# Performance work log

Measured on AMD Instinct MI355X. Metric: run time of the kernel, lower is better.

Reference implementation:

```python
import jax, jax.numpy as jnp
import numpy as np

TAU = 0.8
ALPHA = 0.05
HEBB_LR = 2e-5
NOISE_SCALE = 0.02
SURROGATE = 0.3

@jax.custom_vjp
def spike(v):
    return (v > 0).astype(v.dtype)

def _spike_fwd(v):
    return (v > 0).astype(v.dtype), v

def _spike_bwd(v, g):
    return (g * (SURROGATE * jnp.maximum(1.0 - jnp.abs(v), 0.0)),)

spike.defvjp(_spike_fwd, _spike_bwd)

def setup_inputs() -> dict:
    Nr, B, n = 300, 4, 512
    key = jax.random.key(0)
    ks = jax.random.split(key, 10)
    # distance-decay adjacency, as in build_adjacency (lam=200, coords in a ~500um box)
    coords = jax.random.uniform(ks[0], (Nr, 3)) * 500.0
    D = jnp.linalg.norm(coords[:, None, :] - coords[None, :, :], axis=-1)
    A = 2.0 * jnp.exp(-D / 200.0)
    A = A * (1.0 - jnp.eye(Nr, dtype=A.dtype))          # zero diagonal
    A = A / (A.sum(axis=1, keepdims=True) + 1e-8)       # row-normalize
    W_ff = 0.1 * jax.random.normal(ks[1], (Nr, n, n), dtype=jnp.float32)
    v_s0 = 0.1 * jax.random.normal(ks[2], (Nr, B, n), dtype=jnp.float32)
    v_b0 = 0.1 * jax.random.normal(ks[3], (Nr, B, n), dtype=jnp.float32)
    v_a0 = jnp.zeros((Nr, B, n), dtype=jnp.float32)     # no feedback path -> stays 0
    rbar0 = 0.1 * jax.random.normal(ks[4], (Nr, B, n), dtype=jnp.float32)
    ebar0 = 0.1 * jax.random.normal(ks[5], (Nr, B, n), dtype=jnp.float32)
    noise = jax.random.normal(ks[6], (Nr, B, n), dtype=jnp.float32)
    # visual drive: regions 0 / 1 play the roles of L_R / R_R
    I_L, I_R = 1.2, 1.0
    inp = jnp.zeros((Nr, B, n), dtype=jnp.float32)
    inp = inp.at[0].set(I_L + 0.05 * jax.random.uniform(ks[7], (B, n)))
    inp = inp.at[1].set(I_R + 0.05 * jax.random.uniform(ks[8], (B, n)))
    return {"v_s0": v_s0, "v_b0": v_b0, "v_a0": v_a0, "rbar0": rbar0,
            "ebar0": ebar0, "W_ff": W_ff, "A": A, "inp": inp, "noise": noise}

def reference(v_s0, v_b0, v_a0, rbar0, ebar0, W_ff, A, inp, noise):
    Nr, B, n = v_s0.shape
    # noise injected into every region's v_s BEFORE the region loop
    v_s_all = v_s0 + NOISE_SCALE * noise  # [Nr,B,n]

    # Sequential (Gauss-Seidel) region update: region i sees the already-updated
    # v_s of regions j<i, exactly as the torch double loop does.
    def body(carry, xs):
        i, a_col, vb, va, x_in = xs           # a_col = A[:, i]  [Nr]
        pre = jnp.einsum('j,jbn->bn', a_col, carry)   # adjacency-weighted sum
        x = pre + x_in                                # [B,n]
        pred_b = x @ W_ff[i]                          # [B,n] @ [n,n]
        vb_new = TAU * vb + (1.0 - TAU) * pred_b
        va_new = TAU * va                             # pred_a == 0 (no feedback)
        vs_new = TAU * carry[i] + (1.0 - TAU) * (vb_new - va_new)
        spk = spike(vs_new)
        carry = carry.at[i].set(vs_new)
        return carry, (spk, vb_new, va_new, vs_new, x)

    xs = (jnp.arange(Nr), A.T, v_b0, v_a0, inp)
    _, (spikes, v_b, v_a, v_s, x_all) = jax.lax.scan(body, v_s_all, xs)

    # Hebbian / predictive-coding traces and weight update (no_grad in torch)
    mismatch = v_s - v_b
    rbar = (1.0 - ALPHA) * rbar0 + ALPHA * x_all
    ebar = (1.0 - ALPHA) * ebar0 + ALPHA * mismatch
    dW = jnp.einsum('ibk,ibn->ikn', rbar, ebar) / B
    W_new = W_ff + HEBB_LR * dW

    F = jnp.mean(mismatch ** 2)   # per-region mean of means == global mean (equal sizes)
    return spikes, W_new, F
```

## Files before the change

### kernel.cpp

```cpp
#include <hip/hip_runtime.h>

#define NR   300
#define NB   4
#define NN   512
#define TT   2048
#define CH   30
#define NCH  10
#define SLC  8

#define TAU   0.8f
#define OMT   0.2f
#define ALPH  0.05f
#define OMA   0.95f
#define LRQ   5.0e-6f
#define NSC   0.02f

#define SENT  0xFFFFFFFFu

#define QSTR 136
#define BSTR 544
__device__ __forceinline__ int xidx(int b, int n) {
    return b * BSTR + (n >> 7) * QSTR + (n & 127);
}

__device__ __forceinline__ void ld2_sc_wait(const float* p0, const float* p1,
                                            float4& a, float4& b) {
    asm volatile(
        "global_load_dwordx4 %0, %2, off sc0 sc1\n\t"
        "global_load_dwordx4 %1, %3, off sc0 sc1\n\t"
        "s_waitcnt vmcnt(0)"
        : "=&v"(a), "=&v"(b)
        : "v"(p0), "v"(p1)
        : "memory");
}

__device__ __forceinline__ void ld8_sc_wait(
        const float* p00, const float* p01, const float* p10, const float* p11,
        const float* p20, const float* p21, const float* p30, const float* p31,
        float4& a0, float4& b0, float4& a1, float4& b1,
        float4& a2, float4& b2, float4& a3, float4& b3) {
    asm volatile(
        "global_load_dwordx4 %0, %8, off sc0 sc1\n\t"
        "global_load_dwordx4 %1, %9, off sc0 sc1\n\t"
        "global_load_dwordx4 %2, %10, off sc0 sc1\n\t"
        "global_load_dwordx4 %3, %11, off sc0 sc1\n\t"
        "global_load_dwordx4 %4, %12, off sc0 sc1\n\t"
        "global_load_dwordx4 %5, %13, off sc0 sc1\n\t"
        "global_load_dwordx4 %6, %14, off sc0 sc1\n\t"
        "global_load_dwordx4 %7, %15, off sc0 sc1\n\t"
        "s_waitcnt vmcnt(0)"
        : "=&v"(a0), "=&v"(b0), "=&v"(a1), "=&v"(b1),
          "=&v"(a2), "=&v"(b2), "=&v"(a3), "=&v"(b3)
        : "v"(p00), "v"(p01), "v"(p10), "v"(p11),
          "v"(p20), "v"(p21), "v"(p30), "v"(p31)
        : "memory");
}

__device__ __forceinline__ bool ok8(const float4& a, const float4& b) {
    return __float_as_uint(a.x) != SENT && __float_as_uint(a.y) != SENT &&
           __float_as_uint(a.z) != SENT && __float_as_uint(a.w) != SENT &&
           __float_as_uint(b.x) != SENT && __float_as_uint(b.y) != SENT &&
           __float_as_uint(b.z) != SENT && __float_as_uint(b.w) != SENT;
}

__global__ __launch_bounds__(256) void k_init(const float* __restrict__ vs0,
                                              const float* __restrict__ noise,
                                              float* __restrict__ v_init) {
    int idx = blockIdx.x * 256 + threadIdx.x;
    const float4* a = (const float4*)vs0;
    const float4* b = (const float4*)noise;
    float4* o = (float4*)v_init;
    float4 va = a[idx], vb = b[idx];
    float4 r;
    r.x = va.x + NSC * vb.x; r.y = va.y + NSC * vb.y;
    r.z = va.z + NSC * vb.z; r.w = va.w + NSC * vb.w;
    o[idx] = r;
}

__global__ __launch_bounds__(256) void k_base(const float* __restrict__ A,
                                              const float* __restrict__ v_init,
                                              const float* __restrict__ inp,
                                              float* __restrict__ X) {
    const int i0 = (blockIdx.x >> 1) * 5;
    const int t4 = (blockIdx.x & 1) * 256 + threadIdx.x;
    float4 acc[5];
#pragma unroll
    for (int g = 0; g < 5; g++) acc[g] = make_float4(0.f, 0.f, 0.f, 0.f);
    for (int j = 0; j < NR; j++) {
        const float4 v = ((const float4*)(v_init + (size_t)j * TT))[t4];
#pragma unroll
        for (int g = 0; g < 5; g++) {
            const float a = A[(size_t)j * NR + i0 + g];
            acc[g].x = fmaf(a, v.x, acc[g].x); acc[g].y = fmaf(a, v.y, acc[g].y);
            acc[g].z = fmaf(a, v.z, acc[g].z); acc[g].w = fmaf(a, v.w, acc[g].w);
        }
    }
#pragma unroll
    for (int g = 0; g < 5; g++) {
        const float4 p = ((const float4*)(inp + (size_t)(i0 + g) * TT))[t4];
        float4 r;
        r.x = p.x + acc[g].x; r.y = p.y + acc[g].y;
        r.z = p.z + acc[g].z; r.w = p.w + acc[g].w;
        ((float4*)(X + (size_t)(i0 + g) * TT))[t4] = r;
    }
}

__global__ __launch_bounds__(256, 1) void k_chain(
    const float* __restrict__ W,   const float* __restrict__ vb0,
    const float* __restrict__ va0, const float* __restrict__ A,
    const float* __restrict__ v_init, const float* __restrict__ X,
    const float* __restrict__ rbar0,  const float* __restrict__ ebar0,
    float* __restrict__ delta, int* __restrict__ flagmat,
    float* __restrict__ out_sp, float* __restrict__ outW,
    double* __restrict__ fpart) {

    const int tid  = threadIdx.x;
    const int lane = tid & 63;
    const int wv   = tid >> 6;
    const int rb   = blockIdx.x >> 3;
    const int qq   = blockIdx.x & 7;
    const int k_local = tid >> 2;
    const int mq   = tid & 3;
    const int kg   = qq * 64 + k_local;

    __shared__ __align__(16) float xs[4 * BSTR];
    __shared__ double ps[4];

    const float4* __restrict__ d4 = (const float4*)delta;

    for (int c = 0; c < NCH; c++) {
        const int i = rb + CH * c;
        const size_t base = (size_t)i * TT + (size_t)mq * NN + kg;
        const float vb0v = vb0[base];
        const float va0v = va0[base];
        const float vsi  = v_init[base];
        const float eb0v = ebar0[base];

        float w[128];
        const float* Wp = W + (((size_t)i * NN + (size_t)mq * 128) * NN) + kg;
#pragma unroll
        for (int s = 0; s < 128; s++) w[s] = Wp[(size_t)s * NN];

        float4 r0 = ((const float4*)(X + (size_t)i * TT))[tid];
        float4 r1 = ((const float4*)(X + (size_t)i * TT))[tid + 256];

        int jdone = 0;
        if (i > 0) {
            for (;;) {
                int v = (lane < 32)
                    ? __hip_atomic_load(&flagmat[i * 32 + lane], __ATOMIC_RELAXED, __HIP_MEMORY_SCOPE_AGENT)
                    : 0x7fffffff;
                v = min(v, __shfl_xor(v, 1));
                v = min(v, __shfl_xor(v, 2));
                v = min(v, __shfl_xor(v, 4));
                v = min(v, __shfl_xor(v, 8));
                v = min(v, __shfl_xor(v, 16));
                int r = __shfl(v, 0);
                if (r > i) r = i;
                const bool prog = (r > jdone);
                if (prog) {
                    asm volatile("" ::: "memory");
                    for (int j = jdone; j < r; j++) {
                        const float a = A[(size_t)j * NR + i];
                        const float4 d0 = d4[j * 512 + tid];
                        const float4 d1 = d4[j * 512 + tid + 256];
                        r0.x = fmaf(a, d0.x, r0.x); r0.y = fmaf(a, d0.y, r0.y);
                        r0.z = fmaf(a, d0.z, r0.z); r0.w = fmaf(a, d0.w, r0.w);
                        r1.x = fmaf(a, d1.x, r1.x); r1.y = fmaf(a, d1.y, r1.y);
                        r1.z = fmaf(a, d1.z, r1.z); r1.w = fmaf(a, d1.w, r1.w);
                    }
                    jdone = r;
                }
                const int dist = i - jdone;
                if (dist <= 4) break;
                if (!prog) {
                    if (dist > 24)      __builtin_amdgcn_s_sleep(32);
                    else if (dist > 10) __builtin_amdgcn_s_sleep(8);
                    else                __builtin_amdgcn_s_sleep(1);
                }
            }
            const int n = i - jdone;
            if (n > 0) {
                const int j0 = jdone;
                const int j1 = min(jdone + 1, i - 1);
                const int j2 = min(jdone + 2, i - 1);
                const int j3 = min(jdone + 3, i - 1);
                const float* p00 = delta + (size_t)j0 * TT + 4 * tid;
                const float* p10 = delta + (size_t)j1 * TT + 4 * tid;
                const float* p20 = delta + (size_t)j2 * TT + 4 * tid;
                const float* p30 = delta + (size_t)j3 * TT + 4 * tid;
                float4 a0, b0, a1, b1, a2, b2, a3, b3;
                ld8_sc_wait(p00, p00 + 1024, p10, p10 + 1024,
                            p20, p20 + 1024, p30, p30 + 1024,
                            a0, b0, a1, b1, a2, b2, a3, b3);
#define CONSUME(K, JK, AK, BK, PK)                                             \
                if (K < n) {                                                   \
                    while (!__all(ok8(AK, BK)))                                \
                        ld2_sc_wait(PK, PK + 1024, AK, BK);                    \
                    const float a_ = A[(size_t)JK * NR + i];                   \
                    r0.x = fmaf(a_, AK.x, r0.x); r0.y = fmaf(a_, AK.y, r0.y);  \
                    r0.z = fmaf(a_, AK.z, r0.z); r0.w = fmaf(a_, AK.w, r0.w);  \
                    r1.x = fmaf(a_, BK.x, r1.x); r1.y = fmaf(a_, BK.y, r1.y);  \
                    r1.z = fmaf(a_, BK.z, r1.z); r1.w = fmaf(a_, BK.w, r1.w);  \
                }
                CONSUME(0, j0, a0, b0, p00)
                CONSUME(1, j1, a1, b1, p10)
                CONSUME(2, j2, a2, b2, p20)
                CONSUME(3, j3, a3, b3, p30)
#undef CONSUME
            }
        }

        {
            const int e0 = 4 * tid;
            const int e1 = 4 * tid + 1024;
            *(float4*)&xs[xidx(e0 >> 9, e0 & 511)] = r0;
            *(float4*)&xs[xidx(e1 >> 9, e1 & 511)] = r1;
        }
        __syncthreads();

        float acc0 = 0.f, acc1 = 0.f, acc2 = 0.f, acc3 = 0.f;
#pragma unroll
        for (int s4 = 0; s4 < 32; s4++) {
            const int mb = mq * QSTR + s4 * 4;
            float4 x0 = *(const float4*)&xs[mb];
            float4 x1 = *(const float4*)&xs[BSTR + mb];
            float4 x2 = *(const float4*)&xs[2 * BSTR + mb];
            float4 x3 = *(const float4*)&xs[3 * BSTR + mb];
            const float w0 = w[s4 * 4], w1 = w[s4 * 4 + 1], w2 = w[s4 * 4 + 2], w3 = w[s4 * 4 + 3];
            acc0 += x0.x * w0 + x0.y * w1 + x0.z * w2 + x0.w * w3;
            acc1 += x1.x * w0 + x1.y * w1 + x1.z * w2 + x1.w * w3;
            acc2 += x2.x * w0 + x2.y * w1 + x2.z * w2 + x2.w * w3;
            acc3 += x3.x * w0 + x3.y * w1 + x3.z * w2 + x3.w * w3;
        }
        acc0 += __shfl_xor(acc0, 1); acc0 += __shfl_xor(acc0, 2);
        acc1 += __shfl_xor(acc1, 1); acc1 += __shfl_xor(acc1, 2);
        acc2 += __shfl_xor(acc2, 1); acc2 += __shfl_xor(acc2, 2);
        acc3 += __shfl_xor(acc3, 1); acc3 += __shfl_xor(acc3, 2);
        const float pred = (mq == 0) ? acc0 : (mq == 1) ? acc1 : (mq == 2) ? acc2 : acc3;

        const float vb  = TAU * vb0v + OMT * pred;
        const float va  = TAU * va0v;
        const float vs  = TAU * vsi + OMT * (vb - va);
        __hip_atomic_store(&delta[base], vs - vsi, __ATOMIC_RELAXED, __HIP_MEMORY_SCOPE_AGENT);
        const float mis = vs - vb;

        asm volatile("s_waitcnt vmcnt(0)" ::: "memory");
        {
            const int slot = (qq << 2) + wv;
            for (int r = i + 1 + lane; r < NR; r += 64)
                __hip_atomic_store(&flagmat[r * 32 + slot], i + 1,
                                   __ATOMIC_RELAXED, __HIP_MEMORY_SCOPE_AGENT);
        }
        out_sp[base] = (vs > 0.f) ? 1.f : 0.f;
        __syncthreads();

#pragma unroll
        for (int s = 0; s < 2; s++) {
            const int e = 4 * tid + s * 1024;
            float* xp = &xs[xidx(e >> 9, e & 511)];
            const float4 rr = ((const float4*)(rbar0 + (size_t)i * TT))[tid + s * 256];
            float4 xv = *(float4*)xp;
            xv.x = OMA * rr.x + ALPH * xv.x; xv.y = OMA * rr.y + ALPH * xv.y;
            xv.z = OMA * rr.z + ALPH * xv.z; xv.w = OMA * rr.w + ALPH * xv.w;
            *(float4*)xp = xv;
        }
        __syncthreads();

        const float e_own = OMA * eb0v + ALPH * mis;
        const int qb = lane & ~3;
        const float e0 = __shfl(e_own, qb + 0);
        const float e1 = __shfl(e_own, qb + 1);
        const float e2 = __shfl(e_own, qb + 2);
        const float e3 = __shfl(e_own, qb + 3);

#pragma unroll
        for (int s = 0; s < 128; s++) {
            const int m = mq * 128 + s;
            const int xo = mq * QSTR + s;
            const float dw = e0 * xs[xo] + e1 * xs[BSTR + xo] + e2 * xs[2 * BSTR + xo] + e3 * xs[3 * BSTR + xo];
            outW[(((size_t)i * NN + m) * NN) + kg] = w[s] + LRQ * dw;
        }

        double p = (double)mis * (double)mis;
#pragma unroll
        for (int off = 32; off; off >>= 1) p += __shfl_xor(p, off);
        if (lane == 0) ps[wv] = p;
        __syncthreads();
        if (tid == 0) fpart[(size_t)i * SLC + qq] = ps[0] + ps[1] + ps[2] + ps[3];
        __syncthreads();
    }
}

__global__ __launch_bounds__(256) void k_fin(const double* __restrict__ fpart,
                                             float* __restrict__ outF) {
    __shared__ double ps[256];
    double s = 0.0;
    for (int idx = threadIdx.x; idx < NR * SLC; idx += 256) s += fpart[idx];
    ps[threadIdx.x] = s;
    __syncthreads();
    for (int st = 128; st; st >>= 1) {
        if (threadIdx.x < st) ps[threadIdx.x] += ps[threadIdx.x + st];
        __syncthreads();
    }
    if (threadIdx.x == 0) outF[0] = (float)(ps[0] / 614400.0);
}

extern "C" void kernel_launch(void* const* d_in, const int* in_sizes, int n_in,
                              void* d_out, int out_size, void* d_ws, size_t ws_size,
                              hipStream_t stream) {
    const float* v_s0  = (const float*)d_in[0];
    const float* v_b0  = (const float*)d_in[1];
    const float* v_a0  = (const float*)d_in[2];
    const float* rbar0 = (const float*)d_in[3];
    const float* ebar0 = (const float*)d_in[4];
    const float* W     = (const float*)d_in[5];
    const float* A     = (const float*)d_in[6];
    const float* inp   = (const float*)d_in[7];
    const float* noise = (const float*)d_in[8];

    float* out_sp = (float*)d_out;
    float* out_W  = out_sp + 614400;
    float* out_F  = out_sp + 79257600;

    char* ws = (char*)d_ws;
    float* v_init  = (float*)ws;
    float* X       = v_init + 614400;
    float* delta   = X + 614400;
    int*   flagmat = (int*)(ws + 7372800);
    double* fpart  = (double*)(ws + 7411200);

    (void)hipMemsetAsync(delta, 0xFF, 2457600 + NR * 32 * sizeof(int), stream);
    k_init<<<600, 256, 0, stream>>>(v_s0, noise, v_init);
    k_base<<<120, 256, 0, stream>>>(A, v_init, inp, X);
    k_chain<<<CH * SLC, 256, 0, stream>>>(W, v_b0, v_a0, A, v_init, X,
                                          rbar0, ebar0, delta, flagmat,
                                          out_sp, out_W, fpart);
    k_fin<<<1, 256, 0, stream>>>(fpart, out_F);
}
```

Baseline: 1.282 ms.

## Split each region across 16 blocks of 128 threads instead of 8 of 256

Each region's output columns are now split over 16 blocks of 128 threads, so 480 blocks are launched instead of 240 and more of the GPU's compute units take part in the sequential chain. Each thread now accumulates four float4 chunks of the adjacency sum, and the spin-wait prefetches only the last two predecessor deltas instead of four. The W-update loop reads shared memory as float4 and unrolls by four. The cost is more per-block redundant work on the delta accumulation and X loads, and more cross-block flag traffic. Flag slots still total 32 per region (16 blocks times 2 waves).

```diff
diff --git a/kernel.cpp b/kernel.cpp
--- a/kernel.cpp
+++ b/kernel.cpp
@@ -6,7 +6,7 @@
 #define TT   2048
 #define CH   30
 #define NCH  10
-#define SLC  8
+#define SLC  16
 
 #define TAU   0.8f
 #define OMT   0.2f
@@ -23,22 +23,25 @@
     return b * BSTR + (n >> 7) * QSTR + (n & 127);
 }
 
-__device__ __forceinline__ void ld2_sc_wait(const float* p0, const float* p1,
-                                            float4& a, float4& b) {
+__device__ __forceinline__ void ld4_sc_wait(const float* p0, const float* p1,
+                                            const float* p2, const float* p3,
+                                            float4& a, float4& b, float4& c, float4& d) {
     asm volatile(
-        "global_load_dwordx4 %0, %2, off sc0 sc1\n\t"
-        "global_load_dwordx4 %1, %3, off sc0 sc1\n\t"
+        "global_load_dwordx4 %0, %4, off sc0 sc1\n\t"
+        "global_load_dwordx4 %1, %5, off sc0 sc1\n\t"
+        "global_load_dwordx4 %2, %6, off sc0 sc1\n\t"
+        "global_load_dwordx4 %3, %7, off sc0 sc1\n\t"
         "s_waitcnt vmcnt(0)"
-        : "=&v"(a), "=&v"(b)
-        : "v"(p0), "v"(p1)
+        : "=&v"(a), "=&v"(b), "=&v"(c), "=&v"(d)
+        : "v"(p0), "v"(p1), "v"(p2), "v"(p3)
         : "memory");
 }
 
 __device__ __forceinline__ void ld8_sc_wait(
-        const float* p00, const float* p01, const float* p10, const float* p11,
-        const float* p20, const float* p21, const float* p30, const float* p31,
-        float4& a0, float4& b0, float4& a1, float4& b1,
-        float4& a2, float4& b2, float4& a3, float4& b3) {
+        const float* p00, const float* p01, const float* p02, const float* p03,
+        const float* p10, const float* p11, const float* p12, const float* p13,
+        float4& a0, float4& b0, float4& c0, float4& d0,
+        float4& a1, float4& b1, float4& c1, float4& d1) {
     asm volatile(
         "global_load_dwordx4 %0, %8, off sc0 sc1\n\t"
         "global_load_dwordx4 %1, %9, off sc0 sc1\n\t"
@@ -49,18 +52,20 @@
         "global_load_dwordx4 %6, %14, off sc0 sc1\n\t"
         "global_load_dwordx4 %7, %15, off sc0 sc1\n\t"
         "s_waitcnt vmcnt(0)"
-        : "=&v"(a0), "=&v"(b0), "=&v"(a1), "=&v"(b1),
-          "=&v"(a2), "=&v"(b2), "=&v"(a3), "=&v"(b3)
-        : "v"(p00), "v"(p01), "v"(p10), "v"(p11),
-          "v"(p20), "v"(p21), "v"(p30), "v"(p31)
+        : "=&v"(a0), "=&v"(b0), "=&v"(c0), "=&v"(d0),
+          "=&v"(a1), "=&v"(b1), "=&v"(c1), "=&v"(d1)
+        : "v"(p00), "v"(p01), "v"(p02), "v"(p03),
+          "v"(p10), "v"(p11), "v"(p12), "v"(p13)
         : "memory");
 }
 
-__device__ __forceinline__ bool ok8(const float4& a, const float4& b) {
+__device__ __forceinline__ bool okf4(const float4& a) {
     return __float_as_uint(a.x) != SENT && __float_as_uint(a.y) != SENT &&
-           __float_as_uint(a.z) != SENT && __float_as_uint(a.w) != SENT &&
-           __float_as_uint(b.x) != SENT && __float_as_uint(b.y) != SENT &&
-           __float_as_uint(b.z) != SENT && __float_as_uint(b.w) != SENT;
+           __float_as_uint(a.z) != SENT && __float_as_uint(a.w) != SENT;
+}
+__device__ __forceinline__ bool ok16(const float4& a, const float4& b,
+                                     const float4& c, const float4& d) {
+    return okf4(a) && okf4(b) && okf4(c) && okf4(d);
 }
 
 __global__ __launch_bounds__(256) void k_init(const float* __restrict__ vs0,
@@ -105,7 +110,7 @@
     }
 }
 
-__global__ __launch_bounds__(256, 1) void k_chain(
+__global__ __launch_bounds__(128, 1) void k_chain(
     const float* __restrict__ W,   const float* __restrict__ vb0,
     const float* __restrict__ va0, const float* __restrict__ A,
     const float* __restrict__ v_init, const float* __restrict__ X,
@@ -117,14 +122,14 @@
     const int tid  = threadIdx.x;
     const int lane = tid & 63;
     const int wv   = tid >> 6;
-    const int rb   = blockIdx.x >> 3;
-    const int qq   = blockIdx.x & 7;
+    const int rb   = blockIdx.x >> 4;
+    const int qq   = blockIdx.x & 15;
     const int k_local = tid >> 2;
     const int mq   = tid & 3;
-    const int kg   = qq * 64 + k_local;
+    const int kg   = qq * 32 + k_local;
 
     __shared__ __align__(16) float xs[4 * BSTR];
-    __shared__ double ps[4];
+    __shared__ double ps[2];
 
     const float4* __restrict__ d4 = (const float4*)delta;
 
@@ -142,7 +147,9 @@
         for (int s = 0; s < 128; s++) w[s] = Wp[(size_t)s * NN];
 
         float4 r0 = ((const float4*)(X + (size_t)i * TT))[tid];
-        float4 r1 = ((const float4*)(X + (size_t)i * TT))[tid + 256];
+        float4 r1 = ((const float4*)(X + (size_t)i * TT))[tid + 128];
+        float4 r2 = ((const float4*)(X + (size_t)i * TT))[tid + 256];
+        float4 r3 = ((const float4*)(X + (size_t)i * TT))[tid + 384];
 
         int jdone = 0;
         if (i > 0) {
@@ -163,16 +170,22 @@
                     for (int j = jdone; j < r; j++) {
                         const float a = A[(size_t)j * NR + i];
                         const float4 d0 = d4[j * 512 + tid];
-                        const float4 d1 = d4[j * 512 + tid + 256];
+                        const float4 d1 = d4[j * 512 + tid + 128];
+                        const float4 d2 = d4[j * 512 + tid + 256];
+                        const float4 d3 = d4[j * 512 + tid + 384];
                         r0.x = fmaf(a, d0.x, r0.x); r0.y = fmaf(a, d0.y, r0.y);
                         r0.z = fmaf(a, d0.z, r0.z); r0.w = fmaf(a, d0.w, r0.w);
                         r1.x = fmaf(a, d1.x, r1.x); r1.y = fmaf(a, d1.y, r1.y);
                         r1.z = fmaf(a, d1.z, r1.z); r1.w = fmaf(a, d1.w, r1.w);
+                        r2.x = fmaf(a, d2.x, r2.x); r2.y = fmaf(a, d2.y, r2.y);
+                        r2.z = fmaf(a, d2.z, r2.z); r2.w = fmaf(a, d2.w, r2.w);
+                        r3.x = fmaf(a, d3.x, r3.x); r3.y = fmaf(a, d3.y, r3.y);
+                        r3.z = fmaf(a, d3.z, r3.z); r3.w = fmaf(a, d3.w, r3.w);
                     }
                     jdone = r;
                 }
                 const int dist = i - jdone;
-                if (dist <= 4) break;
+                if (dist <= 2) break;
                 if (!prog) {
                     if (dist > 24)      __builtin_amdgcn_s_sleep(32);
                     else if (dist > 10) __builtin_amdgcn_s_sleep(8);
@@ -183,40 +196,38 @@
             if (n > 0) {
                 const int j0 = jdone;
                 const int j1 = min(jdone + 1, i - 1);
-                const int j2 = min(jdone + 2, i - 1);
-                const int j3 = min(jdone + 3, i - 1);
-                const float* p00 = delta + (size_t)j0 * TT + 4 * tid;
-                const float* p10 = delta + (size_t)j1 * TT + 4 * tid;
-                const float* p20 = delta + (size_t)j2 * TT + 4 * tid;
-                const float* p30 = delta + (size_t)j3 * TT + 4 * tid;
-                float4 a0, b0, a1, b1, a2, b2, a3, b3;
-                ld8_sc_wait(p00, p00 + 1024, p10, p10 + 1024,
-                            p20, p20 + 1024, p30, p30 + 1024,
-                            a0, b0, a1, b1, a2, b2, a3, b3);
-#define CONSUME(K, JK, AK, BK, PK)                                             \
+                const float* p0 = delta + (size_t)j0 * TT + 4 * tid;
+                const float* p1 = delta + (size_t)j1 * TT + 4 * tid;
+                const float aj0 = A[(size_t)j0 * NR + i];
+                const float aj1 = A[(size_t)j1 * NR + i];
+                float4 a0, b0, c0, d0, a1, b1, c1, d1;
+                ld8_sc_wait(p0, p0 + 512, p0 + 1024, p0 + 1536,
+                            p1, p1 + 512, p1 + 1024, p1 + 1536,
+                            a0, b0, c0, d0, a1, b1, c1, d1);
+#define CONSUME(K, AJ, AK, BK, CK, DK, PK)                                     \
                 if (K < n) {                                                   \
-                    while (!__all(ok8(AK, BK)))                                \
-                        ld2_sc_wait(PK, PK + 1024, AK, BK);                    \
-                    const float a_ = A[(size_t)JK * NR + i];                   \
-                    r0.x = fmaf(a_, AK.x, r0.x); r0.y = fmaf(a_, AK.y, r0.y);  \
-                    r0.z = fmaf(a_, AK.z, r0.z); r0.w = fmaf(a_, AK.w, r0.w);  \
-                    r1.x = fmaf(a_, BK.x, r1.x); r1.y = fmaf(a_, BK.y, r1.y);  \
-                    r1.z = fmaf(a_, BK.z, r1.z); r1.w = fmaf(a_, BK.w, r1.w);  \
+                    while (!__all(ok16(AK, BK, CK, DK)))                       \
+                        ld4_sc_wait(PK, PK + 512, PK + 1024, PK + 1536,        \
+                                    AK, BK, CK, DK);                           \
+                    r0.x = fmaf(AJ, AK.x, r0.x); r0.y = fmaf(AJ, AK.y, r0.y);  \
+                    r0.z = fmaf(AJ, AK.z, r0.z); r0.w = fmaf(AJ, AK.w, r0.w);  \
+                    r1.x = fmaf(AJ, BK.x, r1.x); r1.y = fmaf(AJ, BK.y, r1.y);  \
+                    r1.z = fmaf(AJ, BK.z, r1.z); r1.w = fmaf(AJ, BK.w, r1.w);  \
+                    r2.x = fmaf(AJ, CK.x, r2.x); r2.y = fmaf(AJ, CK.y, r2.y);  \
+                    r2.z = fmaf(AJ, CK.z, r2.z); r2.w = fmaf(AJ, CK.w, r2.w);  \
+                    r3.x = fmaf(AJ, DK.x, r3.x); r3.y = fmaf(AJ, DK.y, r3.y);  \
+                    r3.z = fmaf(AJ, DK.z, r3.z); r3.w = fmaf(AJ, DK.w, r3.w);  \
                 }
-                CONSUME(0, j0, a0, b0, p00)
-                CONSUME(1, j1, a1, b1, p10)
-                CONSUME(2, j2, a2, b2, p20)
-                CONSUME(3, j3, a3, b3, p30)
+                CONSUME(0, aj0, a0, b0, c0, d0, p0)
+                CONSUME(1, aj1, a1, b1, c1, d1, p1)
 #undef CONSUME
             }
         }
 
-        {
-            const int e0 = 4 * tid;
-            const int e1 = 4 * tid + 1024;
-            *(float4*)&xs[xidx(e0 >> 9, e0 & 511)] = r0;
-            *(float4*)&xs[xidx(e1 >> 9, e1 & 511)] = r1;
-        }
+        *(float4*)&xs[xidx(0, 4 * tid)] = r0;
+        *(float4*)&xs[xidx(1, 4 * tid)] = r1;
+        *(float4*)&xs[xidx(2, 4 * tid)] = r2;
+        *(float4*)&xs[xidx(3, 4 * tid)] = r3;
         __syncthreads();
 
         float acc0 = 0.f, acc1 = 0.f, acc2 = 0.f, acc3 = 0.f;
@@ -247,7 +258,7 @@
 
         asm volatile("s_waitcnt vmcnt(0)" ::: "memory");
         {
-            const int slot = (qq << 2) + wv;
+            const int slot = (qq << 1) + wv;
             for (int r = i + 1 + lane; r < NR; r += 64)
                 __hip_atomic_store(&flagmat[r * 32 + slot], i + 1,
                                    __ATOMIC_RELAXED, __HIP_MEMORY_SCOPE_AGENT);
@@ -256,10 +267,9 @@
         __syncthreads();
 
 #pragma unroll
-        for (int s = 0; s < 2; s++) {
-            const int e = 4 * tid + s * 1024;
-            float* xp = &xs[xidx(e >> 9, e & 511)];
-            const float4 rr = ((const float4*)(rbar0 + (size_t)i * TT))[tid + s * 256];
+        for (int s = 0; s < 4; s++) {
+            float* xp = &xs[xidx(s, 4 * tid)];
+            const float4 rr = ((const float4*)(rbar0 + (size_t)i * TT))[tid + s * 128];
             float4 xv = *(float4*)xp;
             xv.x = OMA * rr.x + ALPH * xv.x; xv.y = OMA * rr.y + ALPH * xv.y;
             xv.z = OMA * rr.z + ALPH * xv.z; xv.w = OMA * rr.w + ALPH * xv.w;
@@ -275,11 +285,18 @@
         const float e3 = __shfl(e_own, qb + 3);
 
 #pragma unroll
-        for (int s = 0; s < 128; s++) {
-            const int m = mq * 128 + s;
-            const int xo = mq * QSTR + s;
-            const float dw = e0 * xs[xo] + e1 * xs[BSTR + xo] + e2 * xs[2 * BSTR + xo] + e3 * xs[3 * BSTR + xo];
-            outW[(((size_t)i * NN + m) * NN) + kg] = w[s] + LRQ * dw;
+        for (int s4 = 0; s4 < 32; s4++) {
+            const int xo = mq * QSTR + s4 * 4;
+            const float4 X0 = *(const float4*)&xs[xo];
+            const float4 X1 = *(const float4*)&xs[BSTR + xo];
+            const float4 X2 = *(const float4*)&xs[2 * BSTR + xo];
+            const float4 X3 = *(const float4*)&xs[3 * BSTR + xo];
+            const int m0 = mq * 128 + s4 * 4;
+            float* op = &outW[(((size_t)i * NN + m0) * NN) + kg];
+            op[0]      = w[s4*4+0] + LRQ * (e0*X0.x + e1*X1.x + e2*X2.x + e3*X3.x);
+            op[NN]     = w[s4*4+1] + LRQ * (e0*X0.y + e1*X1.y + e2*X2.y + e3*X3.y);
+            op[2*NN]   = w[s4*4+2] + LRQ * (e0*X0.z + e1*X1.z + e2*X2.z + e3*X3.z);
+            op[3*NN]   = w[s4*4+3] + LRQ * (e0*X0.w + e1*X1.w + e2*X2.w + e3*X3.w);
         }
 
         double p = (double)mis * (double)mis;
@@ -287,7 +304,7 @@
         for (int off = 32; off; off >>= 1) p += __shfl_xor(p, off);
         if (lane == 0) ps[wv] = p;
         __syncthreads();
-        if (tid == 0) fpart[(size_t)i * SLC + qq] = ps[0] + ps[1] + ps[2] + ps[3];
+        if (tid == 0) fpart[(size_t)i * SLC + qq] = ps[0] + ps[1];
         __syncthreads();
     }
 }
@@ -333,7 +350,7 @@
     (void)hipMemsetAsync(delta, 0xFF, 2457600 + NR * 32 * sizeof(int), stream);
     k_init<<<600, 256, 0, stream>>>(v_s0, noise, v_init);
     k_base<<<120, 256, 0, stream>>>(A, v_init, inp, X);
-    k_chain<<<CH * SLC, 256, 0, stream>>>(W, v_b0, v_a0, A, v_init, X,
+    k_chain<<<CH * SLC, 128, 0, stream>>>(W, v_b0, v_a0, A, v_init, X,
                                           rbar0, ebar0, delta, flagmat,
                                           out_sp, out_W, fpart);
     k_fin<<<1, 256, 0, stream>>>(fpart, out_F);
```

New measurement: 1.453 ms. +13.4%, slower.
